# Optimization experiments

Hardware: AMD Instinct MI355X
Metric: run time of the kernel (lower is better)

The kernel has to match this reference:

```python
import jax, jax.numpy as jnp
import numpy as np

EPS_NORM = 1e-12   # F.normalize default eps
EPS_ABS = 1e-08


def _l2_normalize(x, axis):
    n = jnp.sqrt(jnp.sum(x * x, axis=axis, keepdims=True))
    return x / jnp.maximum(n, EPS_NORM)


def setup_inputs() -> dict:
    key = jax.random.key(0)
    k1, k2 = jax.random.split(key)
    B, D, H, W = 32, 256, 32, 32
    S = 2048
    features = jax.random.normal(k1, (B, D, H, W), dtype=jnp.float32)
    memory = jax.random.truncated_normal(k2, -2.0, 2.0, (S, D), dtype=jnp.float32) * 0.02
    return {"features": features, "memory": memory}


def reference(features, memory):
    shrink_threshold = 0.0025
    shrink_gamma = 2.0
    temperature = 0.05
    B, D, H, W = features.shape
    S = memory.shape[0]

    # (B,D,H,W) -> (B*H*W, D)
    query = jnp.transpose(features, (0, 2, 3, 1)).reshape(B * H * W, D)

    # addressing: cosine similarity / temperature -> softmax over slots
    q = _l2_normalize(query, axis=1)
    m = _l2_normalize(memory, axis=1)
    sim = (q @ m.T) / temperature                      # [N, S]
    weights = jax.nn.softmax(sim, axis=1)

    # retrieval + soft shrinkage
    retrieved = weights @ memory                       # [N, D]
    a = jnp.abs(retrieved)
    lam = jnp.clip(shrink_gamma * shrink_threshold / (a + EPS_ABS), 0.0, 1.0)
    retrieved = jnp.sign(retrieved) * jax.nn.relu(a * (1.0 - lam))

    # entropy of addressing weights
    entropy = -jnp.mean(jnp.sum(weights * jnp.log(weights + EPS_ABS), axis=1))

    retrieved = jnp.transpose(retrieved.reshape(B, H, W, D), (0, 3, 1, 2))
    weights_image = weights.reshape(B, H * W, S).mean(axis=1)
    return retrieved, entropy, weights_image
```

## Files before the change

kernel.cpp:

```cpp
#include <hip/hip_runtime.h>
#include <cstdint>
#include <cstddef>

#define D_DIM 256
#define S_SLOTS 2048
#define HW_PIX 1024
#define OUT_ENT_IDX 8388608
#define OUT_WIMG_IDX 8388609

#define BUFA_OFF(b) ((b) * 32768)
#define BUFB_OFF(b) (65536 + (b) * 32768)
#define WIMG_OFF    131072
#define DYN_BYTES   139264

using short8 = __attribute__((ext_vector_type(8))) short;
using f32x4  = __attribute__((ext_vector_type(4))) float;

__device__ __forceinline__ unsigned short f2bf(float x) {
    union { float f; unsigned u; } v; v.f = x;
    unsigned r = v.u + 0x7FFF + ((v.u >> 16) & 1);
    return (unsigned short)(r >> 16);
}
__device__ __forceinline__ unsigned pack2(float lo, float hi) {
    return (unsigned)f2bf(lo) | ((unsigned)f2bf(hi) << 16);
}
__device__ __forceinline__ void gload16(const void* g, void* l) {
    __builtin_amdgcn_global_load_lds(
        (const __attribute__((address_space(1))) unsigned int*)g,
        (__attribute__((address_space(3))) unsigned int*)l, 16, 0, 0);
}

__global__ __launch_bounds__(64) void k_prep(const float* __restrict__ mem,
                                             unsigned short* __restrict__ mhatg,
                                             unsigned short* __restrict__ mblkg) {
    __shared__ float lm[8 * 257];
    __shared__ float scl[8];
    const int l = threadIdx.x, blk = blockIdx.x;
    const int tile = blk >> 3, oct = blk & 7;
    const int s0 = tile * 64 + oct * 8;
    const float* src = mem + (size_t)s0 * D_DIM;
#pragma unroll
    for (int i = 0; i < 8; ++i) {
        const int f4 = i * 64 + l;
        const int r = f4 >> 6, dq = (f4 & 63) * 4;
        const float4 v = reinterpret_cast<const float4*>(src)[f4];
        float* p = lm + r * 257 + dq;
        p[0] = v.x; p[1] = v.y; p[2] = v.z; p[3] = v.w;
    }
    __syncthreads();
    {
        const int r = l >> 3, pp = l & 7;
        float ss = 0.f;
#pragma unroll 8
        for (int d = 0; d < 32; ++d) { const float v = lm[r * 257 + pp * 32 + d]; ss += v * v; }
        ss += __shfl_xor(ss, 1); ss += __shfl_xor(ss, 2); ss += __shfl_xor(ss, 4);
        if (pp == 0) scl[r] = 20.0f / fmaxf(sqrtf(ss), 1e-12f);
    }
    __syncthreads();
#pragma unroll
    for (int i = 0; i < 4; ++i) {
        const int c = i * 64 + l, r = c >> 5, k = c & 31;
        const int s_g = s0 + r;
        const float sc = scl[r];
        const float* p = lm + r * 257 + ((k ^ (s_g & 7)) * 8);
        union { short8 s; unsigned short h[8]; } o;
#pragma unroll
        for (int j = 0; j < 8; ++j) o.h[j] = f2bf(p[j] * sc);
        *reinterpret_cast<short8*>((char*)mhatg + (size_t)s_g * 512 + k * 16) = o.s;
    }
#pragma unroll
    for (int i = 0; i < 4; ++i) {
        const int d = i * 64 + l;
        const int k = oct ^ (d & 7);
        union { short8 s; unsigned short h[8]; } o;
#pragma unroll
        for (int j = 0; j < 8; ++j) o.h[j] = f2bf(lm[j * 257 + d]);
        *reinterpret_cast<short8*>((char*)mblkg + (size_t)tile * 32768 + d * 128 + k * 16) = o.s;
    }
}

__device__ __forceinline__ void qkt(const char* mh, const short8 (&qfrag)[2][8],
                                    int srow, int g, int l15, f32x4 (&acc)[2][2]) {
#pragma unroll
    for (int kk = 0; kk < 8; ++kk) {
        const int c0 = ((4 * kk + g) ^ (l15 & 7)) << 4;
        const short8 a0 = *reinterpret_cast<const short8*>(mh + srow * 512 + c0);
        const short8 a1 = *reinterpret_cast<const short8*>(mh + (srow + 16) * 512 + c0);
        acc[0][0] = __builtin_amdgcn_mfma_f32_16x16x32_bf16(a0, qfrag[0][kk], acc[0][0], 0, 0, 0);
        acc[0][1] = __builtin_amdgcn_mfma_f32_16x16x32_bf16(a0, qfrag[1][kk], acc[0][1], 0, 0, 0);
        acc[1][0] = __builtin_amdgcn_mfma_f32_16x16x32_bf16(a1, qfrag[0][kk], acc[1][0], 0, 0, 0);
        acc[1][1] = __builtin_amdgcn_mfma_f32_16x16x32_bf16(a1, qfrag[1][kk], acc[1][1], 0, 0, 0);
    }
}

__global__ __launch_bounds__(512, 2) void k_main(
    const float* __restrict__ feat, const char* __restrict__ mhat_g,
    const char* __restrict__ mblk_g, float* __restrict__ out)
{
    extern __shared__ char dyn[];
    __shared__ float sm_norm[512];
    __shared__ float qs_lds[128];
    __shared__ float zb[2][4][2][16];
    __shared__ float ub[2][4][2][16];
    __shared__ float rZbuf[128];
    __shared__ float entb[4];

    const int tid  = threadIdx.x;
    const int lane = tid & 63;
    const int w    = tid >> 6;
    const int wq   = w & 3;
    const int ws   = w >> 2;
    const int l15  = lane & 15;
    const int g    = (lane >> 4) & 3;
    const int blk  = blockIdx.x;
    const int b    = blk >> 3;
    const int p0   = (blk & 7) * 128;
    const float* fbase = feat + (size_t)b * (D_DIM * HW_PIX);
    float* wimg_l = reinterpret_cast<float*>(dyn + WIMG_OFF);

    auto stageA = [&](int st, int buf) {
        const char* gsrc = mhat_g + (size_t)st * 32768;
        char* ldst = dyn + BUFA_OFF(buf);
#pragma unroll
        for (int i = 0; i < 4; ++i)
            gload16(gsrc + tid * 16 + i * 8192, ldst + tid * 16 + i * 8192);
    };
    auto stageB = [&](int st, int buf) {
        const char* gsrc = mblk_g + (size_t)st * 32768;
        char* ldst = dyn + BUFB_OFF(buf);
#pragma unroll
        for (int i = 0; i < 4; ++i)
            gload16(gsrc + tid * 16 + i * 8192, ldst + tid * 16 + i * 8192);
    };

    stageA(0, 0);

#pragma unroll
    for (int i = 0; i < 4; ++i) wimg_l[i * 512 + tid] = 0.f;

    {
        const int dp = tid >> 7, pp = tid & 127;
        const float* fp = fbase + (size_t)(dp * 64) * HW_PIX + p0 + pp;
        float ss = 0.f;
#pragma unroll 8
        for (int d = 0; d < 64; ++d) { const float v = fp[(size_t)d * HW_PIX]; ss += v * v; }
        sm_norm[dp * 128 + pp] = ss;
    }
    __syncthreads();
    if (tid < 128) {
        const float n2 = sm_norm[tid] + sm_norm[128 + tid] + sm_norm[256 + tid] + sm_norm[384 + tid];
        qs_lds[tid] = 1.0f / fmaxf(sqrtf(n2), 1e-12f);
    }
    __syncthreads();

    short8 qfrag[2][8];
#pragma unroll
    for (int tq = 0; tq < 2; ++tq) {
        const int q = 32 * wq + 16 * tq + l15;
        const float qs = qs_lds[q];
        const float* fq = fbase + p0 + q;
#pragma unroll
        for (int kk = 0; kk < 8; ++kk) {
            union { short8 s; unsigned u[4]; } fr;
#pragma unroll
            for (int jp = 0; jp < 4; ++jp) {
                const int d = 32 * kk + 8 * g + 2 * jp;
                fr.u[jp] = pack2(fq[(size_t)d * HW_PIX] * qs, fq[(size_t)(d + 1) * HW_PIX] * qs);
            }
            qfrag[tq][kk] = fr.s;
        }
    }

    const int srow = 32 * ws + l15;

    float Zp[2] = {0.f, 0.f}, Up[2] = {0.f, 0.f};
    __syncthreads();
    int cur = 0;
    for (int st = 0; st < 32; ++st) {
        if (st < 31) stageA(st + 1, cur ^ 1);
        f32x4 acc[2][2] = {};
        qkt(dyn + BUFA_OFF(cur), qfrag, srow, g, l15, acc);
#pragma unroll
        for (int ts = 0; ts < 2; ++ts)
#pragma unroll
            for (int tq = 0; tq < 2; ++tq)
#pragma unroll
                for (int r = 0; r < 4; ++r) {
                    const float sim = acc[ts][tq][r];
                    const float e = __expf(sim);
                    Zp[tq] += e; Up[tq] += e * sim;
                }
        __syncthreads();
        cur ^= 1;
    }

    stageA(0, 0); stageB(0, 0);

#pragma unroll
    for (int tq = 0; tq < 2; ++tq) {
        Zp[tq] += __shfl_xor(Zp[tq], 16); Zp[tq] += __shfl_xor(Zp[tq], 32);
        Up[tq] += __shfl_xor(Up[tq], 16); Up[tq] += __shfl_xor(Up[tq], 32);
    }
    if (lane < 16) {
#pragma unroll
        for (int tq = 0; tq < 2; ++tq) {
            zb[ws][wq][tq][lane] = Zp[tq];
            ub[ws][wq][tq][lane] = Up[tq];
        }
    }
    __syncthreads();
    float rZ[2], rZw[2];
    {
        float Zf[2], Uf[2];
#pragma unroll
        for (int tq = 0; tq < 2; ++tq) {
            Zf[tq] = Zp[tq] + zb[1 - ws][wq][tq][l15];
            Uf[tq] = Up[tq] + ub[1 - ws][wq][tq][l15];
            rZ[tq] = 1.0f / Zf[tq];
            rZw[tq] = rZ[tq] * (1.0f / 1024.0f);
        }
        if (ws == 0 && lane < 16) {
            rZbuf[32 * wq + l15]      = rZ[0];
            rZbuf[32 * wq + 16 + l15] = rZ[1];
            float ent = 0.f;
#pragma unroll
            for (int tq = 0; tq < 2; ++tq) ent += __logf(Zf[tq]) - Uf[tq] * rZ[tq];
            ent += __shfl_xor(ent, 1); ent += __shfl_xor(ent, 2);
            ent += __shfl_xor(ent, 4); ent += __shfl_xor(ent, 8);
            if (lane == 0) entb[wq] = ent;
        }
    }
    __syncthreads();
    if (tid == 0)
        atomicAdd(out + OUT_ENT_IDX, (entb[0] + entb[1] + entb[2] + entb[3]) * (1.0f / 32768.0f));

    f32x4 acc_o[2][16] = {};
    cur = 0;
    for (int st = 0; st < 32; ++st) {
        if (st < 31) { stageA(st + 1, cur ^ 1); stageB(st + 1, cur ^ 1); }
        f32x4 acc[2][2] = {};
        qkt(dyn + BUFA_OFF(cur), qfrag, srow, g, l15, acc);
        float ev[2][2][4];
#pragma unroll
        for (int ts = 0; ts < 2; ++ts)
#pragma unroll
            for (int tq = 0; tq < 2; ++tq)
#pragma unroll
                for (int r = 0; r < 4; ++r)
                    ev[ts][tq][r] = __expf(acc[ts][tq][r]);

#pragma unroll
        for (int ts = 0; ts < 2; ++ts)
#pragma unroll
            for (int r = 0; r < 4; ++r) {
                float wsum = ev[ts][0][r] * rZw[0] + ev[ts][1][r] * rZw[1];
                wsum += __shfl_xor(wsum, 1);
                wsum += __shfl_xor(wsum, 2);
                wsum += __shfl_xor(wsum, 4);
                wsum += __shfl_xor(wsum, 8);
                if (l15 == 0)
                    atomicAdd(&wimg_l[st * 64 + 32 * ws + 16 * ts + 4 * g + r], wsum);
            }

        short8 pfrag[2];
#pragma unroll
        for (int tq = 0; tq < 2; ++tq) {
            const unsigned u00 = pack2(ev[0][tq][0], ev[0][tq][1]);
            const unsigned u01 = pack2(ev[0][tq][2], ev[0][tq][3]);
            const unsigned u10 = pack2(ev[1][tq][0], ev[1][tq][1]);
            const unsigned u11 = pack2(ev[1][tq][2], ev[1][tq][3]);
            const int sA = l15 + 32 * (g & 1);
            const int sB = sA + 16;
            const unsigned a00 = __shfl((int)u00, sA), a10 = __shfl((int)u10, sA);
            const unsigned a01 = __shfl((int)u01, sA), a11 = __shfl((int)u11, sA);
            const unsigned b00 = __shfl((int)u00, sB), b10 = __shfl((int)u10, sB);
            const unsigned b01 = __shfl((int)u01, sB), b11 = __shfl((int)u11, sB);
            const bool hi = (lane & 32) != 0;
            union { short8 s; unsigned u[4]; } fr;
            fr.u[0] = hi ? a10 : a00;
            fr.u[1] = hi ? a11 : a01;
            fr.u[2] = hi ? b10 : b00;
            fr.u[3] = hi ? b11 : b01;
            pfrag[tq] = fr.s;
        }
        const char* mb = dyn + BUFB_OFF(cur);
        const int cswz = (((4 * ws + g) ^ (l15 & 7)) << 4);
#pragma unroll
        for (int Dt = 0; Dt < 16; ++Dt) {
            const int d = 16 * Dt + l15;
            const short8 bf = *reinterpret_cast<const short8*>(mb + d * 128 + cswz);
            acc_o[0][Dt] = __builtin_amdgcn_mfma_f32_16x16x32_bf16(pfrag[0], bf, acc_o[0][Dt], 0, 0, 0);
            acc_o[1][Dt] = __builtin_amdgcn_mfma_f32_16x16x32_bf16(pfrag[1], bf, acc_o[1][Dt], 0, 0, 0);
        }
        __syncthreads();
        cur ^= 1;
    }

    {
        float* wimg_gb = out + OUT_WIMG_IDX + (size_t)b * S_SLOTS;
#pragma unroll
        for (int i = 0; i < 4; ++i) {
            const int s = i * 512 + tid;
            atomicAdd(wimg_gb + s, wimg_l[s]);
        }
    }

    float rZq[2][4];
#pragma unroll
    for (int tq = 0; tq < 2; ++tq)
#pragma unroll
        for (int r = 0; r < 4; ++r)
            rZq[tq][r] = rZbuf[32 * wq + 16 * tq + 4 * g + r];

#pragma unroll
    for (int Dt = 0; Dt < 16; ++Dt) {
        if (ws == 1) {
#pragma unroll
            for (int tq = 0; tq < 2; ++tq)
                *reinterpret_cast<f32x4*>(dyn + ((wq * 2 + tq) * 64 + lane) * 16) = acc_o[tq][Dt];
        }
        __syncthreads();
        if (ws == 0) {
#pragma unroll
            for (int tq = 0; tq < 2; ++tq) {
                const f32x4 other = *reinterpret_cast<const f32x4*>(dyn + ((wq * 2 + tq) * 64 + lane) * 16);
#pragma unroll
                for (int r = 0; r < 4; ++r) {
                    const float o = (acc_o[tq][Dt][r] + other[r]) * rZq[tq][r];
                    const float a = fabsf(o);
                    const float lam = fminf(0.005f / (a + 1e-8f), 1.0f);
                    const float val = copysignf(a * (1.0f - lam), o);
                    const int q = 32 * wq + 16 * tq + 4 * g + r;
                    *reinterpret_cast<float*>(dyn + 8192 + q * 84 + l15 * 4) = val;
                }
            }
        }
        __syncthreads();
#pragma unroll
        for (int i = 0; i < 4; ++i) {
            const int flat = i * 512 + tid;
            const int dd = flat >> 7, q = flat & 127;
            const float val = *reinterpret_cast<const float*>(dyn + 8192 + q * 84 + dd * 4);
            out[((size_t)b * 256 + Dt * 16 + dd) * HW_PIX + p0 + q] = val;
        }
        __syncthreads();
    }
}

extern "C" void kernel_launch(void* const* d_in, const int* in_sizes, int n_in,
                              void* d_out, int out_size, void* d_ws, size_t ws_size,
                              hipStream_t stream) {
    const float* feat = (const float*)d_in[0];
    const float* mem  = (const float*)d_in[1];
    float* out = (float*)d_out;

    unsigned short* mhat_g = (unsigned short*)d_ws;
    unsigned short* mblk_g = (unsigned short*)((char*)d_ws + (1 << 20));

    hipMemsetAsync((char*)d_out + (size_t)OUT_ENT_IDX * 4, 0,
                   (size_t)(1 + 32 * S_SLOTS) * 4, stream);

    k_prep<<<256, 64, 0, stream>>>(mem, mhat_g, mblk_g);

    hipFuncSetAttribute((const void*)k_main,
                        hipFuncAttributeMaxDynamicSharedMemorySize, DYN_BYTES);
    k_main<<<256, 512, DYN_BYTES, stream>>>(feat, (const char*)mhat_g,
                                            (const char*)mblk_g, out);
}
```

Measured before the change: 241.9 us.

## Split into unnormalized single-pass retrieval kernel plus separate weights-image kernel

The main kernel now computes the softmax denominator and entropy statistics in the same pass as the P·M accumulation, using unnormalized exponentials and normalizing afterwards. This removes the separate first pass over all slots. The per-image weight average needs the final 1/Z, so it moves to a second kernel that recomputes QK^T from the saved reciprocal normalizers. The design relies on the cosine/temperature logits being bounded so that exp without a max-subtraction cannot overflow. The cost is relaunching the query loading, norm computation and QK^T work in a second kernel.

```diff
diff --git a/kernel.cpp b/kernel.cpp
--- a/kernel.cpp
+++ b/kernel.cpp
@@ -10,8 +10,10 @@
 
 #define BUFA_OFF(b) ((b) * 32768)
 #define BUFB_OFF(b) (65536 + (b) * 32768)
-#define WIMG_OFF    131072
-#define DYN_BYTES   139264
+#define FLASH_DYN   131072
+#define WBUFA_OFF(b) ((b) * 32768)
+#define WIMG_OFF     65536
+#define WIMG_DYN     73728
 
 using short8 = __attribute__((ext_vector_type(8))) short;
 using f32x4  = __attribute__((ext_vector_type(4))) float;
@@ -93,9 +95,10 @@
     }
 }
 
-__global__ __launch_bounds__(512, 2) void k_main(
+__global__ __launch_bounds__(512, 2) void k_flash(
     const float* __restrict__ feat, const char* __restrict__ mhat_g,
-    const char* __restrict__ mblk_g, float* __restrict__ out)
+    const char* __restrict__ mblk_g, float* __restrict__ rz_g,
+    float* __restrict__ out)
 {
     extern __shared__ char dyn[];
     __shared__ float sm_norm[512];
@@ -116,7 +119,6 @@
     const int b    = blk >> 3;
     const int p0   = (blk & 7) * 128;
     const float* fbase = feat + (size_t)b * (D_DIM * HW_PIX);
-    float* wimg_l = reinterpret_cast<float*>(dyn + WIMG_OFF);
 
     auto stageA = [&](int st, int buf) {
         const char* gsrc = mhat_g + (size_t)st * 32768;
@@ -133,10 +135,7 @@
             gload16(gsrc + tid * 16 + i * 8192, ldst + tid * 16 + i * 8192);
     };
 
-    stageA(0, 0);
-
-#pragma unroll
-    for (int i = 0; i < 4; ++i) wimg_l[i * 512 + tid] = 0.f;
+    stageA(0, 0); stageB(0, 0);
 
     {
         const int dp = tid >> 7, pp = tid & 127;
@@ -174,68 +173,9 @@
     const int srow = 32 * ws + l15;
 
     float Zp[2] = {0.f, 0.f}, Up[2] = {0.f, 0.f};
+    f32x4 acc_o[2][16] = {};
     __syncthreads();
     int cur = 0;
-    for (int st = 0; st < 32; ++st) {
-        if (st < 31) stageA(st + 1, cur ^ 1);
-        f32x4 acc[2][2] = {};
-        qkt(dyn + BUFA_OFF(cur), qfrag, srow, g, l15, acc);
-#pragma unroll
-        for (int ts = 0; ts < 2; ++ts)
-#pragma unroll
-            for (int tq = 0; tq < 2; ++tq)
-#pragma unroll
-                for (int r = 0; r < 4; ++r) {
-                    const float sim = acc[ts][tq][r];
-                    const float e = __expf(sim);
-                    Zp[tq] += e; Up[tq] += e * sim;
-                }
-        __syncthreads();
-        cur ^= 1;
-    }
-
-    stageA(0, 0); stageB(0, 0);
-
-#pragma unroll
-    for (int tq = 0; tq < 2; ++tq) {
-        Zp[tq] += __shfl_xor(Zp[tq], 16); Zp[tq] += __shfl_xor(Zp[tq], 32);
-        Up[tq] += __shfl_xor(Up[tq], 16); Up[tq] += __shfl_xor(Up[tq], 32);
-    }
-    if (lane < 16) {
-#pragma unroll
-        for (int tq = 0; tq < 2; ++tq) {
-            zb[ws][wq][tq][lane] = Zp[tq];
-            ub[ws][wq][tq][lane] = Up[tq];
-        }
-    }
-    __syncthreads();
-    float rZ[2], rZw[2];
-    {
-        float Zf[2], Uf[2];
-#pragma unroll
-        for (int tq = 0; tq < 2; ++tq) {
-            Zf[tq] = Zp[tq] + zb[1 - ws][wq][tq][l15];
-            Uf[tq] = Up[tq] + ub[1 - ws][wq][tq][l15];
-            rZ[tq] = 1.0f / Zf[tq];
-            rZw[tq] = rZ[tq] * (1.0f / 1024.0f);
-        }
-        if (ws == 0 && lane < 16) {
-            rZbuf[32 * wq + l15]      = rZ[0];
-            rZbuf[32 * wq + 16 + l15] = rZ[1];
-            float ent = 0.f;
-#pragma unroll
-            for (int tq = 0; tq < 2; ++tq) ent += __logf(Zf[tq]) - Uf[tq] * rZ[tq];
-            ent += __shfl_xor(ent, 1); ent += __shfl_xor(ent, 2);
-            ent += __shfl_xor(ent, 4); ent += __shfl_xor(ent, 8);
-            if (lane == 0) entb[wq] = ent;
-        }
-    }
-    __syncthreads();
-    if (tid == 0)
-        atomicAdd(out + OUT_ENT_IDX, (entb[0] + entb[1] + entb[2] + entb[3]) * (1.0f / 32768.0f));
-
-    f32x4 acc_o[2][16] = {};
-    cur = 0;
     for (int st = 0; st < 32; ++st) {
         if (st < 31) { stageA(st + 1, cur ^ 1); stageB(st + 1, cur ^ 1); }
         f32x4 acc[2][2] = {};
@@ -246,21 +186,12 @@
 #pragma unroll
             for (int tq = 0; tq < 2; ++tq)
 #pragma unroll
-                for (int r = 0; r < 4; ++r)
-                    ev[ts][tq][r] = __expf(acc[ts][tq][r]);
-
-#pragma unroll
-        for (int ts = 0; ts < 2; ++ts)
-#pragma unroll
-            for (int r = 0; r < 4; ++r) {
-                float wsum = ev[ts][0][r] * rZw[0] + ev[ts][1][r] * rZw[1];
-                wsum += __shfl_xor(wsum, 1);
-                wsum += __shfl_xor(wsum, 2);
-                wsum += __shfl_xor(wsum, 4);
-                wsum += __shfl_xor(wsum, 8);
-                if (l15 == 0)
-                    atomicAdd(&wimg_l[st * 64 + 32 * ws + 16 * ts + 4 * g + r], wsum);
-            }
+                for (int r = 0; r < 4; ++r) {
+                    const float sim = acc[ts][tq][r];
+                    const float e = __expf(sim);
+                    ev[ts][tq][r] = e;
+                    Zp[tq] += e; Up[tq] += e * sim;
+                }
 
         short8 pfrag[2];
 #pragma unroll
@@ -296,14 +227,43 @@
         cur ^= 1;
     }
 
+#pragma unroll
+    for (int tq = 0; tq < 2; ++tq) {
+        Zp[tq] += __shfl_xor(Zp[tq], 16); Zp[tq] += __shfl_xor(Zp[tq], 32);
+        Up[tq] += __shfl_xor(Up[tq], 16); Up[tq] += __shfl_xor(Up[tq], 32);
+    }
+    if (lane < 16) {
+#pragma unroll
+        for (int tq = 0; tq < 2; ++tq) {
+            zb[ws][wq][tq][lane] = Zp[tq];
+            ub[ws][wq][tq][lane] = Up[tq];
+        }
+    }
+    __syncthreads();
     {
-        float* wimg_gb = out + OUT_WIMG_IDX + (size_t)b * S_SLOTS;
-#pragma unroll
-        for (int i = 0; i < 4; ++i) {
-            const int s = i * 512 + tid;
-            atomicAdd(wimg_gb + s, wimg_l[s]);
-        }
-    }
+        float Zf[2], Uf[2], rZ[2];
+#pragma unroll
+        for (int tq = 0; tq < 2; ++tq) {
+            Zf[tq] = Zp[tq] + zb[1 - ws][wq][tq][l15];
+            Uf[tq] = Up[tq] + ub[1 - ws][wq][tq][l15];
+            rZ[tq] = 1.0f / Zf[tq];
+        }
+        if (ws == 0 && lane < 16) {
+            rZbuf[32 * wq + l15]      = rZ[0];
+            rZbuf[32 * wq + 16 + l15] = rZ[1];
+            rz_g[blk * 128 + 32 * wq + l15]      = rZ[0];
+            rz_g[blk * 128 + 32 * wq + 16 + l15] = rZ[1];
+            float ent = 0.f;
+#pragma unroll
+            for (int tq = 0; tq < 2; ++tq) ent += __logf(Zf[tq]) - Uf[tq] * rZ[tq];
+            ent += __shfl_xor(ent, 1); ent += __shfl_xor(ent, 2);
+            ent += __shfl_xor(ent, 4); ent += __shfl_xor(ent, 8);
+            if (lane == 0) entb[wq] = ent;
+        }
+    }
+    __syncthreads();
+    if (tid == 0)
+        atomicAdd(out + OUT_ENT_IDX, (entb[0] + entb[1] + entb[2] + entb[3]) * (1.0f / 32768.0f));
 
     float rZq[2][4];
 #pragma unroll
@@ -347,6 +307,123 @@
     }
 }
 
+__global__ __launch_bounds__(512, 2) void k_wimg(
+    const float* __restrict__ feat, const char* __restrict__ mhat_g,
+    const float* __restrict__ rz_g, float* __restrict__ out)
+{
+    extern __shared__ char dyn[];
+    __shared__ float sm_norm[512];
+    __shared__ float qs_lds[128];
+
+    const int tid  = threadIdx.x;
+    const int lane = tid & 63;
+    const int w    = tid >> 6;
+    const int wq   = w & 3;
+    const int ws   = w >> 2;
+    const int l15  = lane & 15;
+    const int g    = (lane >> 4) & 3;
+    const int blk  = blockIdx.x;
+    const int b    = blk >> 3;
+    const int p0   = (blk & 7) * 128;
+    const float* fbase = feat + (size_t)b * (D_DIM * HW_PIX);
+    float* wimg_l = reinterpret_cast<float*>(dyn + WIMG_OFF);
+
+    auto stageA = [&](int st, int buf) {
+        const char* gsrc = mhat_g + (size_t)st * 32768;
+        char* ldst = dyn + WBUFA_OFF(buf);
+#pragma unroll
+        for (int i = 0; i < 4; ++i)
+            gload16(gsrc + tid * 16 + i * 8192, ldst + tid * 16 + i * 8192);
+    };
+
+    stageA(0, 0);
+#pragma unroll
+    for (int i = 0; i < 4; ++i) wimg_l[i * 512 + tid] = 0.f;
+
+    {
+        const int dp = tid >> 7, pp = tid & 127;
+        const float* fp = fbase + (size_t)(dp * 64) * HW_PIX + p0 + pp;
+        float ss = 0.f;
+#pragma unroll 8
+        for (int d = 0; d < 64; ++d) { const float v = fp[(size_t)d * HW_PIX]; ss += v * v; }
+        sm_norm[dp * 128 + pp] = ss;
+    }
+    __syncthreads();
+    if (tid < 128) {
+        const float n2 = sm_norm[tid] + sm_norm[128 + tid] + sm_norm[256 + tid] + sm_norm[384 + tid];
+        qs_lds[tid] = 1.0f / fmaxf(sqrtf(n2), 1e-12f);
+    }
+    __syncthreads();
+
+    short8 qfrag[2][8];
+#pragma unroll
+    for (int tq = 0; tq < 2; ++tq) {
+        const int q = 32 * wq + 16 * tq + l15;
+        const float qs = qs_lds[q];
+        const float* fq = fbase + p0 + q;
+#pragma unroll
+        for (int kk = 0; kk < 8; ++kk) {
+            union { short8 s; unsigned u[4]; } fr;
+#pragma unroll
+            for (int jp = 0; jp < 4; ++jp) {
+                const int d = 32 * kk + 8 * g + 2 * jp;
+                fr.u[jp] = pack2(fq[(size_t)d * HW_PIX] * qs, fq[(size_t)(d + 1) * HW_PIX] * qs);
+            }
+            qfrag[tq][kk] = fr.s;
+        }
+    }
+
+    float rzq[2][4];
+#pragma unroll
+    for (int tq = 0; tq < 2; ++tq)
+#pragma unroll
+        for (int r = 0; r < 4; ++r)
+            rzq[tq][r] = rz_g[blk * 128 + 32 * wq + 16 * tq + 4 * g + r] * (1.0f / 1024.0f);
+
+    const int srow = 32 * ws + l15;
+    __syncthreads();
+    int cur = 0;
+    for (int st = 0; st < 32; ++st) {
+        if (st < 31) stageA(st + 1, cur ^ 1);
+        const char* mh = dyn + WBUFA_OFF(cur);
+        f32x4 a2[2][2] = {};
+#pragma unroll
+        for (int kk = 0; kk < 8; ++kk) {
+            const int c0 = ((4 * kk + g) ^ (l15 & 7)) << 4;
+            const short8 m0 = *reinterpret_cast<const short8*>(mh + srow * 512 + c0);
+            const short8 m1 = *reinterpret_cast<const short8*>(mh + (srow + 16) * 512 + c0);
+            a2[0][0] = __builtin_amdgcn_mfma_f32_16x16x32_bf16(qfrag[0][kk], m0, a2[0][0], 0, 0, 0);
+            a2[0][1] = __builtin_amdgcn_mfma_f32_16x16x32_bf16(qfrag[1][kk], m0, a2[0][1], 0, 0, 0);
+            a2[1][0] = __builtin_amdgcn_mfma_f32_16x16x32_bf16(qfrag[0][kk], m1, a2[1][0], 0, 0, 0);
+            a2[1][1] = __builtin_amdgcn_mfma_f32_16x16x32_bf16(qfrag[1][kk], m1, a2[1][1], 0, 0, 0);
+        }
+#pragma unroll
+        for (int sb = 0; sb < 2; ++sb) {
+            float v = 0.f;
+#pragma unroll
+            for (int tq = 0; tq < 2; ++tq)
+#pragma unroll
+                for (int r = 0; r < 4; ++r)
+                    v += __expf(a2[sb][tq][r]) * rzq[tq][r];
+            v += __shfl_xor(v, 16);
+            v += __shfl_xor(v, 32);
+            if (lane < 16)
+                atomicAdd(&wimg_l[st * 64 + 32 * ws + 16 * sb + l15], v);
+        }
+        __syncthreads();
+        cur ^= 1;
+    }
+
+    {
+        float* wimg_gb = out + OUT_WIMG_IDX + (size_t)b * S_SLOTS;
+#pragma unroll
+        for (int i = 0; i < 4; ++i) {
+            const int s = i * 512 + tid;
+            atomicAdd(wimg_gb + s, wimg_l[s]);
+        }
+    }
+}
+
 extern "C" void kernel_launch(void* const* d_in, const int* in_sizes, int n_in,
                               void* d_out, int out_size, void* d_ws, size_t ws_size,
                               hipStream_t stream) {
@@ -356,14 +433,19 @@
 
     unsigned short* mhat_g = (unsigned short*)d_ws;
     unsigned short* mblk_g = (unsigned short*)((char*)d_ws + (1 << 20));
+    float*          rz_g   = (float*)((char*)d_ws + (2 << 20));
 
     hipMemsetAsync((char*)d_out + (size_t)OUT_ENT_IDX * 4, 0,
                    (size_t)(1 + 32 * S_SLOTS) * 4, stream);
 
     k_prep<<<256, 64, 0, stream>>>(mem, mhat_g, mblk_g);
 
-    hipFuncSetAttribute((const void*)k_main,
-                        hipFuncAttributeMaxDynamicSharedMemorySize, DYN_BYTES);
-    k_main<<<256, 512, DYN_BYTES, stream>>>(feat, (const char*)mhat_g,
-                                            (const char*)mblk_g, out);
-}
+    hipFuncSetAttribute((const void*)k_flash,
+                        hipFuncAttributeMaxDynamicSharedMemorySize, FLASH_DYN);
+    k_flash<<<256, 512, FLASH_DYN, stream>>>(feat, (const char*)mhat_g,
+                                             (const char*)mblk_g, rz_g, out);
+
+    hipFuncSetAttribute((const void*)k_wimg,
+                        hipFuncAttributeMaxDynamicSharedMemorySize, WIMG_DYN);
+    k_wimg<<<256, 512, WIMG_DYN, stream>>>(feat, (const char*)mhat_g, rz_g, out);
+}
```

Result: no change. 246.0 us (+1.7%).

## Fuse softmax normalizer pass into retrieval loop and recompute weights for image mean

Applied to the files above, without the earlier changes.

Removes the separate first pass that computed softmax denominators and accumulates Z and the entropy term during the retrieval loop, applying 1/Z afterwards. The per-stage weight-image reduction moves to a trailing pass that recomputes QK^T from a new prepped global layout and scales by 1/Z. Logits are pre-scaled by log2(e) so exp2f replaces expf. This trades one LDS-staged QK pass and the in-loop shuffle-and-atomic reductions for an extra global-memory-fed QK recompute pass.

```diff
diff --git a/kernel.cpp b/kernel.cpp
--- a/kernel.cpp
+++ b/kernel.cpp
@@ -11,7 +11,10 @@
 #define BUFA_OFF(b) ((b) * 32768)
 #define BUFB_OFF(b) (65536 + (b) * 32768)
 #define WIMG_OFF    131072
-#define DYN_BYTES   139264
+#define FUSED_DYN   139264
+
+#define LOG2E_20 28.853900817779268f
+#define LN2F     0.6931471805599453f
 
 using short8 = __attribute__((ext_vector_type(8))) short;
 using f32x4  = __attribute__((ext_vector_type(4))) float;
@@ -32,7 +35,8 @@
 
 __global__ __launch_bounds__(64) void k_prep(const float* __restrict__ mem,
                                              unsigned short* __restrict__ mhatg,
-                                             unsigned short* __restrict__ mblkg) {
+                                             unsigned short* __restrict__ mblkg,
+                                             unsigned short* __restrict__ mqkg) {
     __shared__ float lm[8 * 257];
     __shared__ float scl[8];
     const int l = threadIdx.x, blk = blockIdx.x;
@@ -54,7 +58,7 @@
 #pragma unroll 8
         for (int d = 0; d < 32; ++d) { const float v = lm[r * 257 + pp * 32 + d]; ss += v * v; }
         ss += __shfl_xor(ss, 1); ss += __shfl_xor(ss, 2); ss += __shfl_xor(ss, 4);
-        if (pp == 0) scl[r] = 20.0f / fmaxf(sqrtf(ss), 1e-12f);
+        if (pp == 0) scl[r] = LOG2E_20 / fmaxf(sqrtf(ss), 1e-12f);
     }
     __syncthreads();
 #pragma unroll
@@ -76,6 +80,22 @@
 #pragma unroll
         for (int j = 0; j < 8; ++j) o.h[j] = f2bf(lm[j * 257 + d]);
         *reinterpret_cast<short8*>((char*)mblkg + (size_t)tile * 32768 + d * 128 + k * 16) = o.s;
+    }
+    {
+        const int ws_p = oct >> 2, sb = (oct >> 1) & 1, l15b = (oct & 1) * 8;
+#pragma unroll
+        for (int i = 0; i < 4; ++i) {
+            const int c = i * 64 + l;
+            const int kk = c >> 5, g = (c >> 3) & 3, j = c & 7;
+            const float sc = scl[j];
+            const float* p = lm + j * 257 + (32 * kk + 8 * g);
+            union { short8 s; unsigned short h[8]; } o;
+#pragma unroll
+            for (int t = 0; t < 8; ++t) o.h[t] = f2bf(p[t] * sc);
+            char* dst = (char*)mqkg + (size_t)(((tile * 2 + ws_p) * 8 + kk)) * 2048
+                        + sb * 1024 + (g * 16 + l15b + j) * 16;
+            *reinterpret_cast<short8*>(dst) = o.s;
+        }
     }
 }
 
@@ -93,9 +113,10 @@
     }
 }
 
-__global__ __launch_bounds__(512, 2) void k_main(
+__global__ __launch_bounds__(512, 2) void k_fused(
     const float* __restrict__ feat, const char* __restrict__ mhat_g,
-    const char* __restrict__ mblk_g, float* __restrict__ out)
+    const char* __restrict__ mblk_g, const char* __restrict__ mqk_g,
+    float* __restrict__ out)
 {
     extern __shared__ char dyn[];
     __shared__ float sm_norm[512];
@@ -133,7 +154,7 @@
             gload16(gsrc + tid * 16 + i * 8192, ldst + tid * 16 + i * 8192);
     };
 
-    stageA(0, 0);
+    stageA(0, 0); stageB(0, 0);
 
 #pragma unroll
     for (int i = 0; i < 4; ++i) wimg_l[i * 512 + tid] = 0.f;
@@ -174,68 +195,9 @@
     const int srow = 32 * ws + l15;
 
     float Zp[2] = {0.f, 0.f}, Up[2] = {0.f, 0.f};
+    f32x4 acc_o[2][16] = {};
     __syncthreads();
     int cur = 0;
-    for (int st = 0; st < 32; ++st) {
-        if (st < 31) stageA(st + 1, cur ^ 1);
-        f32x4 acc[2][2] = {};
-        qkt(dyn + BUFA_OFF(cur), qfrag, srow, g, l15, acc);
-#pragma unroll
-        for (int ts = 0; ts < 2; ++ts)
-#pragma unroll
-            for (int tq = 0; tq < 2; ++tq)
-#pragma unroll
-                for (int r = 0; r < 4; ++r) {
-                    const float sim = acc[ts][tq][r];
-                    const float e = __expf(sim);
-                    Zp[tq] += e; Up[tq] += e * sim;
-                }
-        __syncthreads();
-        cur ^= 1;
-    }
-
-    stageA(0, 0); stageB(0, 0);
-
-#pragma unroll
-    for (int tq = 0; tq < 2; ++tq) {
-        Zp[tq] += __shfl_xor(Zp[tq], 16); Zp[tq] += __shfl_xor(Zp[tq], 32);
-        Up[tq] += __shfl_xor(Up[tq], 16); Up[tq] += __shfl_xor(Up[tq], 32);
-    }
-    if (lane < 16) {
-#pragma unroll
-        for (int tq = 0; tq < 2; ++tq) {
-            zb[ws][wq][tq][lane] = Zp[tq];
-            ub[ws][wq][tq][lane] = Up[tq];
-        }
-    }
-    __syncthreads();
-    float rZ[2], rZw[2];
-    {
-        float Zf[2], Uf[2];
-#pragma unroll
-        for (int tq = 0; tq < 2; ++tq) {
-            Zf[tq] = Zp[tq] + zb[1 - ws][wq][tq][l15];
-            Uf[tq] = Up[tq] + ub[1 - ws][wq][tq][l15];
-            rZ[tq] = 1.0f / Zf[tq];
-            rZw[tq] = rZ[tq] * (1.0f / 1024.0f);
-        }
-        if (ws == 0 && lane < 16) {
-            rZbuf[32 * wq + l15]      = rZ[0];
-            rZbuf[32 * wq + 16 + l15] = rZ[1];
-            float ent = 0.f;
-#pragma unroll
-            for (int tq = 0; tq < 2; ++tq) ent += __logf(Zf[tq]) - Uf[tq] * rZ[tq];
-            ent += __shfl_xor(ent, 1); ent += __shfl_xor(ent, 2);
-            ent += __shfl_xor(ent, 4); ent += __shfl_xor(ent, 8);
-            if (lane == 0) entb[wq] = ent;
-        }
-    }
-    __syncthreads();
-    if (tid == 0)
-        atomicAdd(out + OUT_ENT_IDX, (entb[0] + entb[1] + entb[2] + entb[3]) * (1.0f / 32768.0f));
-
-    f32x4 acc_o[2][16] = {};
-    cur = 0;
     for (int st = 0; st < 32; ++st) {
         if (st < 31) { stageA(st + 1, cur ^ 1); stageB(st + 1, cur ^ 1); }
         f32x4 acc[2][2] = {};
@@ -246,22 +208,12 @@
 #pragma unroll
             for (int tq = 0; tq < 2; ++tq)
 #pragma unroll
-                for (int r = 0; r < 4; ++r)
-                    ev[ts][tq][r] = __expf(acc[ts][tq][r]);
-
-#pragma unroll
-        for (int ts = 0; ts < 2; ++ts)
-#pragma unroll
-            for (int r = 0; r < 4; ++r) {
-                float wsum = ev[ts][0][r] * rZw[0] + ev[ts][1][r] * rZw[1];
-                wsum += __shfl_xor(wsum, 1);
-                wsum += __shfl_xor(wsum, 2);
-                wsum += __shfl_xor(wsum, 4);
-                wsum += __shfl_xor(wsum, 8);
-                if (l15 == 0)
-                    atomicAdd(&wimg_l[st * 64 + 32 * ws + 16 * ts + 4 * g + r], wsum);
-            }
-
+                for (int r = 0; r < 4; ++r) {
+                    const float sim2 = acc[ts][tq][r];
+                    const float e = exp2f(sim2);
+                    ev[ts][tq][r] = e;
+                    Zp[tq] += e; Up[tq] += e * sim2;
+                }
         short8 pfrag[2];
 #pragma unroll
         for (int tq = 0; tq < 2; ++tq) {
@@ -296,14 +248,41 @@
         cur ^= 1;
     }
 
-    {
-        float* wimg_gb = out + OUT_WIMG_IDX + (size_t)b * S_SLOTS;
-#pragma unroll
-        for (int i = 0; i < 4; ++i) {
-            const int s = i * 512 + tid;
-            atomicAdd(wimg_gb + s, wimg_l[s]);
-        }
-    }
+#pragma unroll
+    for (int tq = 0; tq < 2; ++tq) {
+        Zp[tq] += __shfl_xor(Zp[tq], 16); Zp[tq] += __shfl_xor(Zp[tq], 32);
+        Up[tq] += __shfl_xor(Up[tq], 16); Up[tq] += __shfl_xor(Up[tq], 32);
+    }
+    if (lane < 16) {
+#pragma unroll
+        for (int tq = 0; tq < 2; ++tq) {
+            zb[ws][wq][tq][lane] = Zp[tq];
+            ub[ws][wq][tq][lane] = Up[tq];
+        }
+    }
+    __syncthreads();
+    {
+        float Zf[2], Uf[2], rZ[2];
+#pragma unroll
+        for (int tq = 0; tq < 2; ++tq) {
+            Zf[tq] = Zp[tq] + zb[1 - ws][wq][tq][l15];
+            Uf[tq] = Up[tq] + ub[1 - ws][wq][tq][l15];
+            rZ[tq] = 1.0f / Zf[tq];
+        }
+        if (ws == 0 && lane < 16) {
+            rZbuf[32 * wq + l15]      = rZ[0];
+            rZbuf[32 * wq + 16 + l15] = rZ[1];
+            float ent = 0.f;
+#pragma unroll
+            for (int tq = 0; tq < 2; ++tq) ent += __logf(Zf[tq]) - LN2F * Uf[tq] * rZ[tq];
+            ent += __shfl_xor(ent, 1); ent += __shfl_xor(ent, 2);
+            ent += __shfl_xor(ent, 4); ent += __shfl_xor(ent, 8);
+            if (lane == 0) entb[wq] = ent;
+        }
+    }
+    __syncthreads();
+    if (tid == 0)
+        atomicAdd(out + OUT_ENT_IDX, (entb[0] + entb[1] + entb[2] + entb[3]) * (1.0f / 32768.0f));
 
     float rZq[2][4];
 #pragma unroll
@@ -345,6 +324,57 @@
         }
         __syncthreads();
     }
+
+    {
+        float rzq[2][4];
+#pragma unroll
+        for (int tq = 0; tq < 2; ++tq)
+#pragma unroll
+            for (int r = 0; r < 4; ++r)
+                rzq[tq][r] = rZbuf[32 * wq + 16 * tq + 4 * g + r] * (1.0f / 1024.0f);
+
+        for (int st = 0; st < 32; ++st) {
+            const char* tb = mqk_g + (size_t)((st * 2 + ws) * 8) * 2048 + lane * 16;
+            f32x4 a2[2][2] = {};
+            short8 mc[2][2];
+            mc[0][0] = *reinterpret_cast<const short8*>(tb);
+            mc[0][1] = *reinterpret_cast<const short8*>(tb + 1024);
+#pragma unroll
+            for (int kk = 0; kk < 8; ++kk) {
+                const int cu2 = kk & 1, nx = cu2 ^ 1;
+                if (kk < 7) {
+                    mc[nx][0] = *reinterpret_cast<const short8*>(tb + (kk + 1) * 2048);
+                    mc[nx][1] = *reinterpret_cast<const short8*>(tb + (kk + 1) * 2048 + 1024);
+                }
+                a2[0][0] = __builtin_amdgcn_mfma_f32_16x16x32_bf16(qfrag[0][kk], mc[cu2][0], a2[0][0], 0, 0, 0);
+                a2[0][1] = __builtin_amdgcn_mfma_f32_16x16x32_bf16(qfrag[1][kk], mc[cu2][0], a2[0][1], 0, 0, 0);
+                a2[1][0] = __builtin_amdgcn_mfma_f32_16x16x32_bf16(qfrag[0][kk], mc[cu2][1], a2[1][0], 0, 0, 0);
+                a2[1][1] = __builtin_amdgcn_mfma_f32_16x16x32_bf16(qfrag[1][kk], mc[cu2][1], a2[1][1], 0, 0, 0);
+            }
+#pragma unroll
+            for (int sb = 0; sb < 2; ++sb) {
+                float v = 0.f;
+#pragma unroll
+                for (int tq = 0; tq < 2; ++tq)
+#pragma unroll
+                    for (int r = 0; r < 4; ++r)
+                        v += exp2f(a2[sb][tq][r]) * rzq[tq][r];
+                v += __shfl_xor(v, 16);
+                v += __shfl_xor(v, 32);
+                if (lane < 16)
+                    atomicAdd(&wimg_l[st * 64 + 32 * ws + 16 * sb + l15], v);
+            }
+        }
+    }
+    __syncthreads();
+    {
+        float* wimg_gb = out + OUT_WIMG_IDX + (size_t)b * S_SLOTS;
+#pragma unroll
+        for (int i = 0; i < 4; ++i) {
+            const int s = i * 512 + tid;
+            atomicAdd(wimg_gb + s, wimg_l[s]);
+        }
+    }
 }
 
 extern "C" void kernel_launch(void* const* d_in, const int* in_sizes, int n_in,
@@ -356,14 +386,16 @@
 
     unsigned short* mhat_g = (unsigned short*)d_ws;
     unsigned short* mblk_g = (unsigned short*)((char*)d_ws + (1 << 20));
+    unsigned short* mqk_g  = (unsigned short*)((char*)d_ws + (2 << 20));
 
     hipMemsetAsync((char*)d_out + (size_t)OUT_ENT_IDX * 4, 0,
                    (size_t)(1 + 32 * S_SLOTS) * 4, stream);
 
-    k_prep<<<256, 64, 0, stream>>>(mem, mhat_g, mblk_g);
-
-    hipFuncSetAttribute((const void*)k_main,
-                        hipFuncAttributeMaxDynamicSharedMemorySize, DYN_BYTES);
-    k_main<<<256, 512, DYN_BYTES, stream>>>(feat, (const char*)mhat_g,
-                                            (const char*)mblk_g, out);
-}
+    k_prep<<<256, 64, 0, stream>>>(mem, mhat_g, mblk_g, mqk_g);
+
+    hipFuncSetAttribute((const void*)k_fused,
+                        hipFuncAttributeMaxDynamicSharedMemorySize, FUSED_DYN);
+    k_fused<<<256, 512, FUSED_DYN, stream>>>(feat, (const char*)mhat_g,
+                                             (const char*)mblk_g,
+                                             (const char*)mqk_g, out);
+}
```

New measurement: 284.8 us. 1.18x slower.
